# Kernel optimization log

Hardware: AMD Instinct MI355X
Metric: run time of the kernel (lower is better)

The kernel has to match this reference:

```python
import jax, jax.numpy as jnp
import numpy as np

NUM_HEADS = 16
DIM_HEAD = 64
SCALE = DIM_HEAD ** -0.5


def setup_inputs() -> dict:
    key = jax.random.key(0)
    k1, k2, k3 = jax.random.split(key, 3)
    b, s, h = 2, 2048, 1024
    x = jax.random.normal(k1, (b, s, h), dtype=jnp.float32)
    w_qkv = jax.random.normal(k2, (3 * h, h), dtype=jnp.float32) * (h ** -0.5)
    w_out = jax.random.normal(k3, (h, h), dtype=jnp.float32) * (h ** -0.5)
    b_out = jnp.zeros((h,), dtype=jnp.float32)
    return {"x": x, "w_qkv": w_qkv, "w_out": w_out, "b_out": b_out}


def reference(x, w_qkv, w_out, b_out):
    b, s, hid = x.shape
    # qkv projection (no bias): [b, s, 3*hid]
    qkv = jnp.einsum('bsh,oh->bso', x, w_qkv)
    # split order in original rearrange is (qkv, heads, dim_head)
    qkv = qkv.reshape(b, s, 3, NUM_HEADS, DIM_HEAD)
    q = jnp.transpose(qkv[:, :, 0], (0, 2, 1, 3))  # [b, H, s, d]
    k = jnp.transpose(qkv[:, :, 1], (0, 2, 1, 3))
    v = jnp.transpose(qkv[:, :, 2], (0, 2, 1, 3))
    # naive attention: full [b, H, s, s] score matrix, as in the source
    att = jnp.einsum('bhxd,bhyd->bhxy', q, k) * SCALE
    att = jax.nn.softmax(att, axis=-1)
    out = jnp.einsum('bhxy,bhyd->bhxd', att, v)  # [b, H, s, d]
    out = jnp.transpose(out, (0, 2, 1, 3)).reshape(b, s, NUM_HEADS * DIM_HEAD)
    return jnp.einsum('bsi,oi->bso', out, w_out) + b_out
```

## Files before the change

kernel.cpp:

```cpp
#include <hip/hip_runtime.h>
#include <hip/hip_bf16.h>

#define B_ 2
#define S_ 2048
#define HID 1024
#define NH 16
#define DH 64
#define QKV_N (3*HID)
#define M_ROWS (B_*S_)

typedef __attribute__((ext_vector_type(8))) short short8;
typedef __attribute__((ext_vector_type(4))) short short4v;
typedef __attribute__((ext_vector_type(4))) float floatx4;
typedef __attribute__((ext_vector_type(4))) unsigned int uint4v;
typedef unsigned int uint;

#define QSCALE 0.18033688f

__device__ __forceinline__ short8 load8(const __hip_bfloat16* p) {
    return *(const short8*)p;
}

#if __has_builtin(__builtin_amdgcn_exp2f)
#define EXP2F(x) __builtin_amdgcn_exp2f(x)
#else
#define EXP2F(x) exp2f(x)
#endif

__device__ __forceinline__ uint pack_bf16_2(float lo, float hi) {
    uint ul = __float_as_uint(lo) + 0x8000u;
    uint uh = __float_as_uint(hi) + 0x8000u;
    return __builtin_amdgcn_perm(uh, ul, 0x07060302);
}
__device__ __forceinline__ uint pack_bf16_2_rtne(float lo, float hi) {
    uint ul = __float_as_uint(lo); ul += 0x7FFFu + ((ul >> 16) & 1u);
    uint uh = __float_as_uint(hi); uh += 0x7FFFu + ((uh >> 16) & 1u);
    return __builtin_amdgcn_perm(uh, ul, 0x07060302);
}

#define ASYNC16(gptr, lptr) \
    __builtin_amdgcn_global_load_lds((const __attribute__((address_space(1))) void*)(gptr), \
                                     (__attribute__((address_space(3))) void*)(lptr), 16, 0, 0)
#define RAW_BARRIER() asm volatile("s_barrier" ::: "memory")

__global__ __launch_bounds__(256) void cvt_all(
    const float* __restrict__ x, const float* __restrict__ wq,
    const float* __restrict__ wo, __hip_bfloat16* __restrict__ out)
{
    const int n0 = M_ROWS * HID, n1 = QKV_N * HID;
    int i = (blockIdx.x * 256 + threadIdx.x) * 4;
    const float* src; int off;
    if (i < n0)           { src = x;  off = i; }
    else if (i < n0 + n1) { src = wq; off = i - n0; }
    else                  { src = wo; off = i - n0 - n1; }
    float4 v = *(const float4*)(src + off);
    uint2 r;
    r.x = pack_bf16_2_rtne(v.x, v.y);
    r.y = pack_bf16_2_rtne(v.z, v.w);
    *(uint2*)(out + i) = r;
}

#define BK 32
#define NITER 32
template<int MODE, int TMB>
__global__ __launch_bounds__(256, (TMB == 128) ? 3 : 4) void gemm_bt_kernel(
    const __hip_bfloat16* __restrict__ A,
    const __hip_bfloat16* __restrict__ Bw,
    const float* __restrict__ biasf,
    __hip_bfloat16* __restrict__ C,
    float* __restrict__ Cf,
    __hip_bfloat16* __restrict__ VT,
    int Mdim, int Ndim, int Kdim)
{
    constexpr int NI = TMB / 32;
    constexpr int CA = TMB / 64;
    constexpr int WAITG = 0x0F70 | (CA + 2);
    __shared__ alignas(16) __hip_bfloat16 As[3][TMB * BK];
    __shared__ alignas(16) __hip_bfloat16 Bs[3][128 * BK];

    const int tid  = threadIdx.x;
    const int wave = tid >> 6;
    const int lane = tid & 63;
    const int q = lane >> 4;
    const int r = lane & 15;
    const int m_blk = blockIdx.y * TMB;
    const int n_blk = blockIdx.x * 128;
    const int wm = (wave >> 1) * (TMB / 2);
    const int wn = (wave & 1) * 64;

    const __hip_bfloat16* Abase = A + (size_t)m_blk * Kdim;
    const __hip_bfloat16* Bbase = Bw + (size_t)n_blk * Kdim;

    floatx4 acc[NI][4];
#pragma unroll
    for (int i = 0; i < NI; i++)
#pragma unroll
        for (int j = 0; j < 4; j++) acc[i][j] = (floatx4){0.f, 0.f, 0.f, 0.f};

    auto stage = [&](int bf, int kt) {
#pragma unroll
        for (int c = 0; c < CA; c++) {
            int ch = tid + c * 256;
            ASYNC16(Abase + (size_t)(ch >> 2) * Kdim + kt + (ch & 3) * 8, &As[bf][ch * 8]);
        }
#pragma unroll
        for (int c = 0; c < 2; c++) {
            int ch = tid + c * 256;
            ASYNC16(Bbase + (size_t)(ch >> 2) * Kdim + kt + (ch & 3) * 8, &Bs[bf][ch * 8]);
        }
    };
    auto compute = [&](int bf) {
        short8 a[NI], b[4];
#pragma unroll
        for (int i = 0; i < NI; i++) a[i] = *(const short8*)&As[bf][(wm + i * 16 + r) * BK + q * 8];
#pragma unroll
        for (int j = 0; j < 4; j++) b[j] = *(const short8*)&Bs[bf][(wn + j * 16 + r) * BK + q * 8];
#pragma unroll
        for (int i = 0; i < NI; i++)
#pragma unroll
            for (int j = 0; j < 4; j++)
                acc[i][j] = __builtin_amdgcn_mfma_f32_16x16x32_bf16(b[j], a[i], acc[i][j], 0, 0, 0);
    };

    stage(0, 0);
    stage(1, BK);
#pragma unroll 3
    for (int it = 0; it < NITER - 2; it++) {
        __builtin_amdgcn_s_waitcnt(WAITG);
        RAW_BARRIER();
        stage((it + 2) % 3, (it + 2) * BK);
        compute(it % 3);
    }
    __builtin_amdgcn_s_waitcnt(WAITG);
    RAW_BARRIER();
    compute((NITER - 2) % 3);
    __builtin_amdgcn_s_waitcnt(0x0F70);
    RAW_BARRIER();
    compute((NITER - 1) % 3);

#pragma unroll
    for (int i = 0; i < NI; i++) {
        const int m = m_blk + wm + i * 16 + r;
#pragma unroll
        for (int j = 0; j < 4; j++) {
            const int n0 = n_blk + wn + j * 16 + q * 4;
            if (MODE == 2) {
                float4 bv = *(const float4*)&biasf[n0];
                float4 ov;
                ov.x = acc[i][j][0] + bv.x;
                ov.y = acc[i][j][1] + bv.y;
                ov.z = acc[i][j][2] + bv.z;
                ov.w = acc[i][j][3] + bv.w;
                *(float4*)&Cf[(size_t)m * Ndim + n0] = ov;
            } else if (n_blk < 2 * HID) {
                float s = (n0 < HID) ? QSCALE : 1.0f;
                uint2 pk;
                pk.x = pack_bf16_2_rtne(acc[i][j][0] * s, acc[i][j][1] * s);
                pk.y = pack_bf16_2_rtne(acc[i][j][2] * s, acc[i][j][3] * s);
                *(uint2*)&C[(size_t)m * QKV_N + n0] = pk;
            } else {
                int bidx = m >> 11;
                int srow = m & (S_ - 1);
                int c = srow & 31;
                int sp = (srow & ~31) | (((c >> 2) & 3) << 3) | (((c >> 4) & 1) << 2) | (c & 3);
#pragma unroll
                for (int reg = 0; reg < 4; reg++) {
                    int dfull = n0 + reg - 2 * HID;
                    VT[((size_t)bidx * HID + dfull) * S_ + sp] =
                        __float2bfloat16(acc[i][j][reg]);
                }
            }
        }
    }
}

#define KT 32

__global__ __launch_bounds__(512, 4) void flash_kernel(
    const __hip_bfloat16* __restrict__ qkv,
    const __hip_bfloat16* __restrict__ VTp,
    __hip_bfloat16* __restrict__ O)
{
    __shared__ alignas(16) char smem[49152];
    __hip_bfloat16* lds_k = (__hip_bfloat16*)smem;
    __hip_bfloat16* lds_v = (__hip_bfloat16*)(smem + 24576);

    const int tid  = threadIdx.x;
    const int wave = tid >> 6;
    const int lane = tid & 63;
    const int q = lane >> 4;
    const int r = lane & 15;
    const int ww   = wave & 3;
    const int khid = wave >> 2;
    const int bh = blockIdx.x;
    const int b  = bh >> 4;
    const int h  = bh & 15;
    const int s0 = blockIdx.y * 128 + ww * 32;

    const __hip_bfloat16* Qbase = qkv + (size_t)b * S_ * QKV_N + h * DH;
    const __hip_bfloat16* Kbase = Qbase + HID;
    const __hip_bfloat16* Vbase = VTp + ((size_t)b * HID + h * DH) * S_;

    const int sr = ww * 8 + (lane >> 3);
    const int kcg = (lane & 7) ^ ((lane >> 3) & 7);
    const __hip_bfloat16* gK = Kbase + (size_t)(khid * 1024 + sr) * QKV_N + kcg * 8;
    const int kldso = sr * 64 + (lane & 7) * 8;
    const int vr = ww * 16 + (lane >> 2);
    const int fv = (vr + (vr >> 2)) & 3;
    const int vcg = (lane & 3) ^ fv;
    const __hip_bfloat16* gV = Vbase + (size_t)vr * S_ + khid * 1024 + vcg * 8;
    const int vldso = vr * 32 + (lane & 3) * 8;

    auto stage = [&](int bf, int it) {
        ASYNC16(gK + (size_t)(it * KT) * QKV_N, &lds_k[(bf * 2 + khid) * 2048 + kldso]);
        ASYNC16(gV + it * KT,                   &lds_v[(bf * 2 + khid) * 2048 + vldso]);
    };

    floatx4 o_acc[2][4];
    floatx4 l_acc[2];
#pragma unroll
    for (int rt = 0; rt < 2; rt++) {
        l_acc[rt] = (floatx4){0.f, 0.f, 0.f, 0.f};
#pragma unroll
        for (int nb = 0; nb < 4; nb++) o_acc[rt][nb] = (floatx4){0.f, 0.f, 0.f, 0.f};
    }
    short8 ones;
#pragma unroll
    for (int i = 0; i < 8; i++) ones[i] = (short)0x3F80;

    short8 a_q[2][2];
    auto compute = [&](int bf) {
        const __hip_bfloat16* Kt = &lds_k[(bf * 2 + khid) * 2048];
        const __hip_bfloat16* Vt = &lds_v[(bf * 2 + khid) * 2048];
        short8 bk[2][2];
#pragma unroll
        for (int ct = 0; ct < 2; ct++)
#pragma unroll
            for (int kh = 0; kh < 2; kh++)
                bk[ct][kh] = *(const short8*)&Kt[(ct * 16 + r) * 64 + ((kh * 4 + q) ^ (r & 7)) * 8];
        short8 vb[4];
#pragma unroll
        for (int nb = 0; nb < 4; nb++) {
            int d = nb * 16 + r;
            vb[nb] = *(const short8*)&Vt[d * 32 + ((q ^ ((d + (d >> 2)) & 3)) * 8)];
        }

#pragma unroll
        for (int rt = 0; rt < 2; rt++) {
            floatx4 sc[2];
#pragma unroll
            for (int ct = 0; ct < 2; ct++) {
                floatx4 z = (floatx4){0.f, 0.f, 0.f, 0.f};
                z = __builtin_amdgcn_mfma_f32_16x16x32_bf16(bk[ct][0], a_q[rt][0], z, 0, 0, 0);
                z = __builtin_amdgcn_mfma_f32_16x16x32_bf16(bk[ct][1], a_q[rt][1], z, 0, 0, 0);
                sc[ct] = z;
            }
            uint4v up;
            up.x = pack_bf16_2(EXP2F(sc[0][0]), EXP2F(sc[0][1]));
            up.y = pack_bf16_2(EXP2F(sc[0][2]), EXP2F(sc[0][3]));
            up.z = pack_bf16_2(EXP2F(sc[1][0]), EXP2F(sc[1][1]));
            up.w = pack_bf16_2(EXP2F(sc[1][2]), EXP2F(sc[1][3]));
            short8 pa = __builtin_bit_cast(short8, up);

            __builtin_amdgcn_s_setprio(1);
            l_acc[rt] = __builtin_amdgcn_mfma_f32_16x16x32_bf16(pa, ones, l_acc[rt], 0, 0, 0);
#pragma unroll
            for (int nb = 0; nb < 4; nb++)
                o_acc[rt][nb] = __builtin_amdgcn_mfma_f32_16x16x32_bf16(pa, vb[nb], o_acc[rt][nb], 0, 0, 0);
            __builtin_amdgcn_s_setprio(0);
        }
    };

    auto step = [&](int it, int bf) {
        __builtin_amdgcn_s_waitcnt(0x0F72);
        RAW_BARRIER();
        stage((bf + 2) % 3, it + 2);
        compute(bf);
    };

    stage(0, 0);
#pragma unroll
    for (int rt = 0; rt < 2; rt++)
#pragma unroll
        for (int kh = 0; kh < 2; kh++)
            a_q[rt][kh] = load8(Qbase + (size_t)(s0 + rt * 16 + r) * QKV_N + kh * 32 + q * 8);
    __builtin_amdgcn_s_waitcnt(0x0F70);
    stage(1, 1);

    for (int itb = 0; itb < 30; itb += 3) {
        step(itb + 0, 0);
        step(itb + 1, 1);
        step(itb + 2, 2);
    }
    __builtin_amdgcn_s_waitcnt(0x0F72);
    RAW_BARRIER();
    compute(0);
    __builtin_amdgcn_s_waitcnt(0x0F70);
    RAW_BARRIER();
    compute(1);

    __syncthreads();
    float* of = (float*)smem;
    float* lf = (float*)(smem + 32768);
    if (khid == 1) {
#pragma unroll
        for (int rt = 0; rt < 2; rt++) {
#pragma unroll
            for (int nb = 0; nb < 4; nb++)
                *(floatx4*)&of[ww * 2048 + (rt * 4 + nb) * 256 + lane * 4] = o_acc[rt][nb];
            *(floatx4*)&lf[ww * 512 + rt * 256 + lane * 4] = l_acc[rt];
        }
    }
    __syncthreads();
    if (khid == 0) {
#pragma unroll
        for (int rt = 0; rt < 2; rt++) {
            l_acc[rt] += *(const floatx4*)&lf[ww * 512 + rt * 256 + lane * 4];
#pragma unroll
            for (int nb = 0; nb < 4; nb++)
                o_acc[rt][nb] += *(const floatx4*)&of[ww * 2048 + (rt * 4 + nb) * 256 + lane * 4];
        }
#pragma unroll
        for (int rt = 0; rt < 2; rt++) {
#pragma unroll
            for (int reg = 0; reg < 4; reg++) {
                float inv = 1.f / l_acc[rt][reg];
                int srow2 = s0 + rt * 16 + q * 4 + reg;
                __hip_bfloat16* Orow = O + ((size_t)b * S_ + srow2) * HID + h * DH;
#pragma unroll
                for (int nb = 0; nb < 4; nb++)
                    Orow[nb * 16 + r] = __float2bfloat16(o_acc[rt][nb][reg] * inv);
            }
        }
    }
}

extern "C" void kernel_launch(void* const* d_in, const int* in_sizes, int n_in,
                              void* d_out, int out_size, void* d_ws, size_t ws_size,
                              hipStream_t stream) {
    const float* x_f     = (const float*)d_in[0];
    const float* w_qkv_f = (const float*)d_in[1];
    const float* w_out_f = (const float*)d_in[2];
    const float* b_out_f = (const float*)d_in[3];
    float* out = (float*)d_out;

    __hip_bfloat16* xb      = (__hip_bfloat16*)d_ws;
    __hip_bfloat16* wqkvb   = xb    + (size_t)M_ROWS * HID;
    __hip_bfloat16* woutb   = wqkvb + (size_t)QKV_N * HID;
    __hip_bfloat16* qkv_ws  = woutb + (size_t)HID * HID;
    __hip_bfloat16* vt_ws   = qkv_ws + (size_t)M_ROWS * QKV_N;
    __hip_bfloat16* attn_ws = vt_ws + (size_t)B_ * HID * S_;

    dim3 blk(256);
    {
        int ntot = M_ROWS * HID + QKV_N * HID + HID * HID;
        cvt_all<<<dim3(ntot / 1024), blk, 0, stream>>>(x_f, w_qkv_f, w_out_f, xb);
    }

    gemm_bt_kernel<1, 128><<<dim3(QKV_N / 128, M_ROWS / 128), blk, 0, stream>>>(
        xb, wqkvb, nullptr, qkv_ws, nullptr, vt_ws, M_ROWS, QKV_N, HID);
    flash_kernel<<<dim3(B_ * NH, S_ / 128), dim3(512), 0, stream>>>(qkv_ws, vt_ws, attn_ws);
    gemm_bt_kernel<2, 64><<<dim3(HID / 128, M_ROWS / 64), blk, 0, stream>>>(
        attn_ws, woutb, b_out_f, nullptr, out, nullptr, M_ROWS, HID, HID);
}
```

Measured before the change: 175.9 us.

## Halve flash block to 4 waves, each wave covering 64 query rows

The flash attention block drops from 8 waves to 4. Each wave now processes 4 query row-tiles (64 rows) instead of 2, so every K/V fragment read from LDS feeds twice as many MFMAs. Each thread issues two async K and two async V loads per stage, and the waitcnt thresholds are adjusted to match. The cost is higher register pressure from the doubled accumulators and fewer waves per block to hide latency.

```diff
diff --git a/kernel.cpp b/kernel.cpp
--- a/kernel.cpp
+++ b/kernel.cpp
@@ -176,7 +176,7 @@
 
 #define KT 32
 
-__global__ __launch_bounds__(512, 4) void flash_kernel(
+__global__ __launch_bounds__(256, 2) void flash_kernel(
     const __hip_bfloat16* __restrict__ qkv,
     const __hip_bfloat16* __restrict__ VTp,
     __hip_bfloat16* __restrict__ O)
@@ -190,36 +190,47 @@
     const int lane = tid & 63;
     const int q = lane >> 4;
     const int r = lane & 15;
-    const int ww   = wave & 3;
-    const int khid = wave >> 2;
+    const int qg   = wave >> 1;
+    const int khid = wave & 1;
+    const int khs  = wave >> 1;
     const int bh = blockIdx.x;
     const int b  = bh >> 4;
     const int h  = bh & 15;
-    const int s0 = blockIdx.y * 128 + ww * 32;
+    const int s0 = blockIdx.y * 128 + qg * 64;
 
     const __hip_bfloat16* Qbase = qkv + (size_t)b * S_ * QKV_N + h * DH;
     const __hip_bfloat16* Kbase = Qbase + HID;
     const __hip_bfloat16* Vbase = VTp + ((size_t)b * HID + h * DH) * S_;
 
-    const int sr = ww * 8 + (lane >> 3);
+    const int sr0 = (wave & 1) * 16 + (lane >> 3);
+    const int sr1 = sr0 + 8;
     const int kcg = (lane & 7) ^ ((lane >> 3) & 7);
-    const __hip_bfloat16* gK = Kbase + (size_t)(khid * 1024 + sr) * QKV_N + kcg * 8;
-    const int kldso = sr * 64 + (lane & 7) * 8;
-    const int vr = ww * 16 + (lane >> 2);
-    const int fv = (vr + (vr >> 2)) & 3;
-    const int vcg = (lane & 3) ^ fv;
-    const __hip_bfloat16* gV = Vbase + (size_t)vr * S_ + khid * 1024 + vcg * 8;
-    const int vldso = vr * 32 + (lane & 3) * 8;
+    const __hip_bfloat16* gK0 = Kbase + (size_t)(khs * 1024 + sr0) * QKV_N + kcg * 8;
+    const __hip_bfloat16* gK1 = Kbase + (size_t)(khs * 1024 + sr1) * QKV_N + kcg * 8;
+    const int kldso0 = sr0 * 64 + (lane & 7) * 8;
+    const int kldso1 = sr1 * 64 + (lane & 7) * 8;
+    const int vr0 = (wave & 1) * 32 + (lane >> 2);
+    const int vr1 = vr0 + 16;
+    const int fv0 = (vr0 + (vr0 >> 2)) & 3;
+    const int fv1 = (vr1 + (vr1 >> 2)) & 3;
+    const int vcg0 = (lane & 3) ^ fv0;
+    const int vcg1 = (lane & 3) ^ fv1;
+    const __hip_bfloat16* gV0 = Vbase + (size_t)vr0 * S_ + khs * 1024 + vcg0 * 8;
+    const __hip_bfloat16* gV1 = Vbase + (size_t)vr1 * S_ + khs * 1024 + vcg1 * 8;
+    const int vldso0 = vr0 * 32 + (lane & 3) * 8;
+    const int vldso1 = vr1 * 32 + (lane & 3) * 8;
 
     auto stage = [&](int bf, int it) {
-        ASYNC16(gK + (size_t)(it * KT) * QKV_N, &lds_k[(bf * 2 + khid) * 2048 + kldso]);
-        ASYNC16(gV + it * KT,                   &lds_v[(bf * 2 + khid) * 2048 + vldso]);
-    };
-
-    floatx4 o_acc[2][4];
-    floatx4 l_acc[2];
-#pragma unroll
-    for (int rt = 0; rt < 2; rt++) {
+        ASYNC16(gK0 + (size_t)(it * KT) * QKV_N, &lds_k[(bf * 2 + khs) * 2048 + kldso0]);
+        ASYNC16(gK1 + (size_t)(it * KT) * QKV_N, &lds_k[(bf * 2 + khs) * 2048 + kldso1]);
+        ASYNC16(gV0 + it * KT,                   &lds_v[(bf * 2 + khs) * 2048 + vldso0]);
+        ASYNC16(gV1 + it * KT,                   &lds_v[(bf * 2 + khs) * 2048 + vldso1]);
+    };
+
+    floatx4 o_acc[4][4];
+    floatx4 l_acc[4];
+#pragma unroll
+    for (int rt = 0; rt < 4; rt++) {
         l_acc[rt] = (floatx4){0.f, 0.f, 0.f, 0.f};
 #pragma unroll
         for (int nb = 0; nb < 4; nb++) o_acc[rt][nb] = (floatx4){0.f, 0.f, 0.f, 0.f};
@@ -228,7 +239,7 @@
 #pragma unroll
     for (int i = 0; i < 8; i++) ones[i] = (short)0x3F80;
 
-    short8 a_q[2][2];
+    short8 a_q[4][2];
     auto compute = [&](int bf) {
         const __hip_bfloat16* Kt = &lds_k[(bf * 2 + khid) * 2048];
         const __hip_bfloat16* Vt = &lds_v[(bf * 2 + khid) * 2048];
@@ -246,7 +257,7 @@
         }
 
 #pragma unroll
-        for (int rt = 0; rt < 2; rt++) {
+        for (int rt = 0; rt < 4; rt++) {
             floatx4 sc[2];
 #pragma unroll
             for (int ct = 0; ct < 2; ct++) {
@@ -272,7 +283,7 @@
     };
 
     auto step = [&](int it, int bf) {
-        __builtin_amdgcn_s_waitcnt(0x0F72);
+        __builtin_amdgcn_s_waitcnt(0x0F74);
         RAW_BARRIER();
         stage((bf + 2) % 3, it + 2);
         compute(bf);
@@ -280,7 +291,7 @@
 
     stage(0, 0);
 #pragma unroll
-    for (int rt = 0; rt < 2; rt++)
+    for (int rt = 0; rt < 4; rt++)
 #pragma unroll
         for (int kh = 0; kh < 2; kh++)
             a_q[rt][kh] = load8(Qbase + (size_t)(s0 + rt * 16 + r) * QKV_N + kh * 32 + q * 8);
@@ -292,7 +303,7 @@
         step(itb + 1, 1);
         step(itb + 2, 2);
     }
-    __builtin_amdgcn_s_waitcnt(0x0F72);
+    __builtin_amdgcn_s_waitcnt(0x0F74);
     RAW_BARRIER();
     compute(0);
     __builtin_amdgcn_s_waitcnt(0x0F70);
@@ -304,24 +315,24 @@
     float* lf = (float*)(smem + 32768);
     if (khid == 1) {
 #pragma unroll
-        for (int rt = 0; rt < 2; rt++) {
+        for (int rt = 0; rt < 4; rt++) {
 #pragma unroll
             for (int nb = 0; nb < 4; nb++)
-                *(floatx4*)&of[ww * 2048 + (rt * 4 + nb) * 256 + lane * 4] = o_acc[rt][nb];
-            *(floatx4*)&lf[ww * 512 + rt * 256 + lane * 4] = l_acc[rt];
+                *(floatx4*)&of[qg * 4096 + (rt * 4 + nb) * 256 + lane * 4] = o_acc[rt][nb];
+            *(floatx4*)&lf[qg * 1024 + rt * 256 + lane * 4] = l_acc[rt];
         }
     }
     __syncthreads();
     if (khid == 0) {
 #pragma unroll
-        for (int rt = 0; rt < 2; rt++) {
-            l_acc[rt] += *(const floatx4*)&lf[ww * 512 + rt * 256 + lane * 4];
+        for (int rt = 0; rt < 4; rt++) {
+            l_acc[rt] += *(const floatx4*)&lf[qg * 1024 + rt * 256 + lane * 4];
 #pragma unroll
             for (int nb = 0; nb < 4; nb++)
-                o_acc[rt][nb] += *(const floatx4*)&of[ww * 2048 + (rt * 4 + nb) * 256 + lane * 4];
-        }
-#pragma unroll
-        for (int rt = 0; rt < 2; rt++) {
+                o_acc[rt][nb] += *(const floatx4*)&of[qg * 4096 + (rt * 4 + nb) * 256 + lane * 4];
+        }
+#pragma unroll
+        for (int rt = 0; rt < 4; rt++) {
 #pragma unroll
             for (int reg = 0; reg < 4; reg++) {
                 float inv = 1.f / l_acc[rt][reg];
@@ -359,7 +370,7 @@
 
     gemm_bt_kernel<1, 128><<<dim3(QKV_N / 128, M_ROWS / 128), blk, 0, stream>>>(
         xb, wqkvb, nullptr, qkv_ws, nullptr, vt_ws, M_ROWS, QKV_N, HID);
-    flash_kernel<<<dim3(B_ * NH, S_ / 128), dim3(512), 0, stream>>>(qkv_ws, vt_ws, attn_ws);
+    flash_kernel<<<dim3(B_ * NH, S_ / 128), dim3(256), 0, stream>>>(qkv_ws, vt_ws, attn_ws);
     gemm_bt_kernel<2, 64><<<dim3(HID / 128, M_ROWS / 64), blk, 0, stream>>>(
         attn_ws, woutb, b_out_f, nullptr, out, nullptr, M_ROWS, HID, HID);
 }
```

New measurement: 179.2 us. About the same (+1.9%).
